# Kernel optimization log

Hardware: AMD Instinct MI355X
Metric: run time of the kernel (lower is better)

The kernel has to match this reference:

```python
import jax, jax.numpy as jnp
import numpy as np

I, H, NH, A = 128, 2048, 2, 4   # input_size, hidden_size, n_hidden, alpha_dim
K = 2 * A * A                   # per-position theta entries
B = 8192


def make_masks():
    # MADE sequential-ordering masks, identical to DART.create_masks
    inp = np.arange(I)
    degrees = [inp] + [np.arange(H) % (I - 1) for _ in range(NH + 1)] + [np.arange(I) - 1]
    masks = [(d1[:, None] >= d0[None, :]).astype(np.float32)
             for d0, d1 in zip(degrees[:-1], degrees[1:])]
    # last mask repeated per theta entry: repeat(1, K).view(-1, H) == row-repeat
    masks[-1] = np.repeat(masks[-1], K, axis=0)
    return [jnp.asarray(m) for m in masks]


def setup_inputs() -> dict:
    key = jax.random.key(0)
    ks = jax.random.split(key, 5)
    x = jax.random.normal(ks[0], (B, I), dtype=jnp.float32)

    def lin(k, out_dim, in_dim):
        kw, kb = jax.random.split(k)
        s = 1.0 / np.sqrt(in_dim)
        W = jax.random.uniform(kw, (out_dim, in_dim), minval=-s, maxval=s, dtype=jnp.float32)
        b = jax.random.uniform(kb, (out_dim,), minval=-s, maxval=s, dtype=jnp.float32)
        return W, b

    W0, b0 = lin(ks[1], H, I)
    W1, b1 = lin(ks[2], H, H)
    W2, b2 = lin(ks[3], H, H)
    W3, b3 = lin(ks[4], I * K, H)
    return dict(x=x, W0=W0, b0=b0, W1=W1, b1=b1, W2=W2, b2=b2, W3=W3, b3=b3)


def logexpmm(a, b):
    # log-domain matmul: out[..., i, j] = logsumexp_k(a[..., i, k] + b[..., k, j])
    return jax.nn.logsumexp(a[..., :, :, None] + b[..., None, :, :], axis=-2)


def reference(x, W0, b0, W1, b1, W2, b2, W3, b3):
    m = make_masks()
    h = jax.nn.relu(x @ (m[0] * W0).T + b0)
    h = jax.nn.relu(h @ (m[1] * W1).T + b1)
    h = jax.nn.relu(h @ (m[2] * W2).T + b2)
    theta = (h @ (m[3] * W3).T + b3).reshape(-1, I, 2, A, A)
    mu, alpha = theta[:, :, 0], theta[:, :, 1]  # (B, I, A, A)

    LOG2PI = float(np.log(2.0 * np.pi))
    xe = x[:, :, None, None]
    # Normal(mu, exp(alpha)).log_prob(x) - log(alpha_dim)
    logp = (-0.5 * ((xe - mu) * jnp.exp(-alpha)) ** 2
            - alpha - 0.5 * LOG2PI - jnp.log(jnp.float32(A)))

    first = logp[:, 0, 0:1]        # (B, 1, A)
    last = logp[:, -1, :, 0:1]     # (B, A, 1)
    inner = jnp.swapaxes(logp[:, 1:-1], 0, 1)  # (I-2, B, A, A)

    def step(carry, mtx):
        return logexpmm(carry, mtx), None

    prod, _ = jax.lax.scan(step, inner[0], inner[1:])
    return logexpmm(first, logexpmm(prod, last))  # (B, 1, 1)
```

## Files before the change

kernel.cpp:

```cpp
#include <hip/hip_runtime.h>
#include <hip/hip_bf16.h>
#include <cstdint>
#include <cstddef>

#define AS1 __attribute__((address_space(1)))
#define AS3 __attribute__((address_space(3)))

typedef __bf16 bf16x8  __attribute__((ext_vector_type(8)));
typedef float  floatx4 __attribute__((ext_vector_type(4)));

__device__ __forceinline__ void load_lds16(const void* g, void* l) {
    __builtin_amdgcn_global_load_lds((AS1 void*)g, (AS3 void*)l, 16, 0, 0);
}

__device__ __forceinline__ float fexp2(float x) { return __builtin_amdgcn_exp2f(x); }
__device__ __forceinline__ float flog2(float x) { return __builtin_amdgcn_logf(x); }

#define LOG2E 1.4426950408889634f
#define LN2   0.6931471805599453f
#define C0K   2.3052328943245633f

__device__ __forceinline__ float logp2(float xv, float mu, float al) {
    float e = fexp2(-al * LOG2E);
    float z = (xv - mu) * e;
    return (-0.5f * z * z - al - C0K) * LOG2E;
}
__device__ __forceinline__ float lse4(float a0, float a1, float a2, float a3) {
    float mx = fmaxf(fmaxf(a0, a1), fmaxf(a2, a3));
    return mx + flog2(fexp2(a0 - mx) + fexp2(a1 - mx) +
                      fexp2(a2 - mx) + fexp2(a3 - mx));
}
__device__ __forceinline__ void lmm4(const float* Aa, const float* Bb, float* D) {
#pragma unroll
    for (int r = 0; r < 4; ++r)
#pragma unroll
        for (int c = 0; c < 4; ++c)
            D[r * 4 + c] = lse4(Aa[r * 4 + 0] + Bb[0 * 4 + c],
                                Aa[r * 4 + 1] + Bb[1 * 4 + c],
                                Aa[r * 4 + 2] + Bb[2 * 4 + c],
                                Aa[r * 4 + 3] + Bb[3 * 4 + c]);
}

__device__ __forceinline__ int resp_s(int p) {
    return p < 272 ? p / 17 : 16 + ((p - 272) >> 4);
}
__device__ __forceinline__ int invp_s(int p) {
    if (p < 272) { int d = p / 17; int r = p - d * 17;
                   return r < 16 ? d + r * 127 : 2032 + d; }
    int d = 16 + ((p - 272) >> 4); int j = (p - 272) & 15;
    return d + j * 127;
}
__device__ __forceinline__ int cnt_le(int D) {
    return D < 16 ? (D + 1) * 17 : 272 + ((D - 15) << 4);
}

__global__ __launch_bounds__(256)
void prep_all(const float* __restrict__ x,  const float* __restrict__ W0,
              const float* __restrict__ W1, const float* __restrict__ W2,
              const float* __restrict__ W3,
              __bf16* __restrict__ xb,  __bf16* __restrict__ w0m,
              __bf16* __restrict__ w1m, __bf16* __restrict__ w2m,
              __bf16* __restrict__ w3m)
{
    __shared__ float lds[2048];
    const int blk = blockIdx.x;
    const int tid = threadIdx.x;
    const int t8  = tid * 8;

    if (blk < 640) {
        bf16x8 o;
        if (blk < 512) {
            size_t base = (size_t)blk * 2048 + t8;
            floatx4 a = *(const floatx4*)(x + base);
            floatx4 b = *(const floatx4*)(x + base + 4);
#pragma unroll
            for (int j = 0; j < 4; ++j) { o[j] = (__bf16)a[j]; o[4 + j] = (__bf16)b[j]; }
            *(bf16x8*)(xb + base) = o;
        } else {
            long idx = (long)(blk - 512) * 2048 + t8;
            int p_n = (int)(idx >> 7);
            int c   = (int)(idx & 127);
            int dg  = resp_s(p_n);
            const float* s = W0 + (long)invp_s(p_n) * 128 + c;
            floatx4 a = *(const floatx4*)s;
            floatx4 b = *(const floatx4*)(s + 4);
#pragma unroll
            for (int j = 0; j < 8; ++j) {
                float v = j < 4 ? a[j] : b[j - 4];
                o[j] = (__bf16)((dg >= c + j) ? v : 0.0f);
            }
            *(bf16x8*)(w0m + idx) = o;
        }
        return;
    }

    const float* srow; __bf16* drow; int deg_n; bool strict;
    if (blk < 2688) {
        int p_n = blk - 640;
        srow = W1 + (size_t)invp_s(p_n) * 2048; drow = w1m + (size_t)p_n * 2048;
        deg_n = resp_s(p_n); strict = false;
    } else if (blk < 4736) {
        int p_n = blk - 2688;
        srow = W2 + (size_t)invp_s(p_n) * 2048; drow = w2m + (size_t)p_n * 2048;
        deg_n = resp_s(p_n); strict = false;
    } else {
        int n = blk - 4736;
        srow = W3 + (size_t)n * 2048; drow = w3m + (size_t)n * 2048;
        deg_n = n >> 5; strict = true;
    }
    floatx4 a = *(const floatx4*)(srow + t8);
    floatx4 b = *(const floatx4*)(srow + t8 + 4);
    *(floatx4*)&lds[t8]     = a;
    *(floatx4*)&lds[t8 + 4] = b;
    __syncthreads();
    bf16x8 o;
#pragma unroll
    for (int j = 0; j < 8; ++j) {
        int p = t8 + j;
        float v = lds[invp_s(p)];
        int dg = resp_s(p);
        bool keep = strict ? (deg_n > dg) : (deg_n >= dg);
        o[j] = (__bf16)(keep ? v : 0.0f);
    }
    *(bf16x8*)(drow + t8) = o;
}

template <bool RELU, bool OBF16, bool TLAYOUT, bool PERMBIAS, int LMODE>
__global__ __launch_bounds__(256, 4)
void gemm_bt(const __bf16* __restrict__ A, const __bf16* __restrict__ Bw,
             const float* __restrict__ bias, void* __restrict__ Cout,
             int N, int K)
{
    __shared__ __align__(16) __bf16 lsA[128 * 64];
    __shared__ __align__(16) __bf16 lsB[128 * 64];
    const int tid  = threadIdx.x;
    const int wave = tid >> 6;
    const int lane = tid & 63;
    const int bm = blockIdx.x;
    const int bn = (gridDim.y - 1) - blockIdx.y;
    const int wm = wave >> 1, wn = wave & 1;

    const int r8 = lane >> 3;
    const int cb = (lane & 7) ^ r8;
    const __bf16* gsrc[8];
    __bf16* ldst[8];
#pragma unroll
    for (int t = 0; t < 8; ++t) {
        int j = wave * 8 + t;
        if (j < 16) {
            int row = bm * 128 + j * 8 + r8;
            gsrc[t] = A + (size_t)row * K + cb * 8;
            ldst[t] = lsA + j * 512;
        } else {
            int jj = j - 16;
            int row = bn * 128 + jj * 8 + r8;
            gsrc[t] = Bw + (size_t)row * K + cb * 8;
            ldst[t] = lsB + jj * 512;
        }
    }

    const int fr  = lane & 15;
    const int ks  = lane >> 4;
    const int sx  = fr & 7;
    const int sl0 = ((ks)     ^ sx) * 8;
    const int sl1 = ((4 + ks) ^ sx) * 8;
    const __bf16* arow[4];
    const __bf16* brow[4];
#pragma unroll
    for (int i = 0; i < 4; ++i) {
        arow[i] = lsA + (wm * 64 + i * 16 + fr) * 64;
        brow[i] = lsB + (wn * 64 + i * 16 + fr) * 64;
    }

    floatx4 acc[4][4];
    const floatx4 vzero = {0.f, 0.f, 0.f, 0.f};
#pragma unroll
    for (int mi = 0; mi < 4; ++mi)
#pragma unroll
        for (int ni = 0; ni < 4; ++ni) acc[mi][ni] = vzero;

    const int nk = K >> 6;
    int limit;
    if (LMODE == 0)      limit = (cnt_le(resp_s(bn * 128 + 127)) + 63) >> 6;
    else if (LMODE == 1) { int D = 4 * bn + 2; if (D > 126) D = 126;
                           limit = (cnt_le(D) + 63) >> 6; }
    else                 limit = (resp_s(bn * 128 + 127) + 64) >> 6;
    if (limit > nk) limit = nk;

    for (int it = 0; it < limit; ++it) {
        const int kt = it << 6;
        __syncthreads();
#pragma unroll
        for (int t = 0; t < 8; ++t)
            load_lds16((const void*)(gsrc[t] + kt), (void*)ldst[t]);
        __syncthreads();
        bf16x8 af[4], bf[4];
#pragma unroll
        for (int i = 0; i < 4; ++i) af[i] = *(const bf16x8*)(arow[i] + sl0);
#pragma unroll
        for (int i = 0; i < 4; ++i) bf[i] = *(const bf16x8*)(brow[i] + sl0);
#pragma unroll
        for (int mi = 0; mi < 4; ++mi)
#pragma unroll
            for (int ni = 0; ni < 4; ++ni)
                acc[mi][ni] = __builtin_amdgcn_mfma_f32_16x16x32_bf16(
                    af[mi], bf[ni], acc[mi][ni], 0, 0, 0);
#pragma unroll
        for (int i = 0; i < 4; ++i) af[i] = *(const bf16x8*)(arow[i] + sl1);
#pragma unroll
        for (int i = 0; i < 4; ++i) bf[i] = *(const bf16x8*)(brow[i] + sl1);
#pragma unroll
        for (int mi = 0; mi < 4; ++mi)
#pragma unroll
            for (int ni = 0; ni < 4; ++ni)
                acc[mi][ni] = __builtin_amdgcn_mfma_f32_16x16x32_bf16(
                    af[mi], bf[ni], acc[mi][ni], 0, 0, 0);
    }

    const int cn  = lane & 15;
    const int cr4 = (lane >> 4) * 4;
#pragma unroll
    for (int ni = 0; ni < 4; ++ni) {
        int col = bn * 128 + wn * 64 + ni * 16 + cn;
        float bv = bias[PERMBIAS ? invp_s(col) : col];
#pragma unroll
        for (int mi = 0; mi < 4; ++mi) {
            int row0 = bm * 128 + wm * 64 + mi * 16 + cr4;
#pragma unroll
            for (int q = 0; q < 4; ++q) {
                float v = acc[mi][ni][q] + bv;
                if (RELU) v = fmaxf(v, 0.f);
                if (TLAYOUT) {
                    size_t addr = (size_t)(bm * 2 + wm) * ((size_t)N * 64)
                                + (size_t)col * 64 + (mi * 16 + cr4 + q);
                    ((__bf16*)Cout)[addr] = (__bf16)v;
                } else if (OBF16) {
                    ((__bf16*)Cout)[(size_t)(row0 + q) * N + col] = (__bf16)v;
                } else {
                    ((float*)Cout)[(size_t)(row0 + q) * N + col] = v;
                }
            }
        }
    }
}

#define CFENCE() asm volatile("" ::: "memory")
#define BARX()  do { CFENCE(); __builtin_amdgcn_s_barrier(); CFENCE(); } while (0)
#define WVM2()  asm volatile("s_waitcnt vmcnt(2)" ::: "memory")
#define WVM0()  asm volatile("s_waitcnt vmcnt(0)" ::: "memory")
#define WLGK()  asm volatile("s_waitcnt lgkmcnt(0)" ::: "memory")

template <bool RELU, bool OBF16, bool TLAYOUT, bool PERMBIAS, int LMODE>
__global__ __launch_bounds__(512)
void gemm8p(const __bf16* __restrict__ A, const __bf16* __restrict__ Bw,
            const float* __restrict__ bias, void* __restrict__ Cout,
            int N, int K)
{
    __shared__ __align__(16) __bf16 ls[2 * 24576];
    const int tid  = threadIdx.x;
    const int wave = tid >> 6;
    const int lane = tid & 63;
    const int bm = blockIdx.x;
    const int bn = (gridDim.y - 1) - blockIdx.y;
    const int wm = wave >> 1, wn = wave & 1;

    const int l8 = lane >> 3;
    const int cb = (lane & 7) ^ l8;
    const __bf16* gA[2][2];  int dA[2][2];
    const __bf16* gB[2];     int dB[2];
#pragma unroll
    for (int h = 0; h < 2; ++h)
#pragma unroll
        for (int s = 0; s < 2; ++s) {
            int rt = h * 128 + wave * 16 + s * 8;
            gA[h][s] = A + (size_t)(bm * 256 + rt + l8) * K + cb * 8;
            dA[h][s] = rt * 64;
        }
#pragma unroll
    for (int s = 0; s < 2; ++s) {
        int rt = wave * 16 + s * 8;
        gB[s] = Bw + (size_t)(bn * 128 + rt + l8) * K + cb * 8;
        dB[s] = 16384 + rt * 64;
    }

#define STG_A(buf, kt) do { \
    load_lds16((const void*)(gA[0][0] + (kt)), (void*)(ls + (buf)*24576 + dA[0][0])); \
    load_lds16((const void*)(gA[0][1] + (kt)), (void*)(ls + (buf)*24576 + dA[0][1])); \
    load_lds16((const void*)(gA[1][0] + (kt)), (void*)(ls + (buf)*24576 + dA[1][0])); \
    load_lds16((const void*)(gA[1][1] + (kt)), (void*)(ls + (buf)*24576 + dA[1][1])); } while (0)
#define STG_B(buf, kt) do { \
    load_lds16((const void*)(gB[0] + (kt)), (void*)(ls + (buf)*24576 + dB[0])); \
    load_lds16((const void*)(gB[1] + (kt)), (void*)(ls + (buf)*24576 + dB[1])); } while (0)

    const int fr  = lane & 15;
    const int ks  = lane >> 4;
    const int sx  = fr & 7;
    const int sl0 = ((ks)     ^ sx) * 8;
    const int sl1 = ((4 + ks) ^ sx) * 8;
    int aoff[4], boff[4];
#pragma unroll
    for (int i = 0; i < 4; ++i) {
        aoff[i] = (wm * 64 + i * 16 + fr) * 64;
        boff[i] = 16384 + (wn * 64 + i * 16 + fr) * 64;
    }

    floatx4 acc[4][4];
    const floatx4 vzero = {0.f, 0.f, 0.f, 0.f};
#pragma unroll
    for (int mi = 0; mi < 4; ++mi)
#pragma unroll
        for (int ni = 0; ni < 4; ++ni) acc[mi][ni] = vzero;

    bf16x8 bfr[4][2], afr[2][2];

#define DSRD_B(buf) do { \
    _Pragma("unroll") \
    for (int ni = 0; ni < 4; ++ni) { \
        bfr[ni][0] = *(const bf16x8*)(ls + (buf)*24576 + boff[ni] + sl0); \
        bfr[ni][1] = *(const bf16x8*)(ls + (buf)*24576 + boff[ni] + sl1); } } while (0)
#define DSRD_A(buf, q) do { \
    _Pragma("unroll") \
    for (int j = 0; j < 2; ++j) { \
        afr[j][0] = *(const bf16x8*)(ls + (buf)*24576 + aoff[2*(q)+j] + sl0); \
        afr[j][1] = *(const bf16x8*)(ls + (buf)*24576 + aoff[2*(q)+j] + sl1); } } while (0)
#define MFMA16(q) do { \
    __builtin_amdgcn_s_setprio(1); \
    _Pragma("unroll") \
    for (int j = 0; j < 2; ++j) \
    _Pragma("unroll") \
    for (int ni = 0; ni < 4; ++ni) { \
        acc[2*(q)+j][ni] = __builtin_amdgcn_mfma_f32_16x16x32_bf16( \
            afr[j][0], bfr[ni][0], acc[2*(q)+j][ni], 0, 0, 0); \
        acc[2*(q)+j][ni] = __builtin_amdgcn_mfma_f32_16x16x32_bf16( \
            afr[j][1], bfr[ni][1], acc[2*(q)+j][ni], 0, 0, 0); } \
    __builtin_amdgcn_s_setprio(0); } while (0)

    const int nk = K >> 6;
    int limit;
    if (LMODE == 0)      limit = (cnt_le(resp_s(bn * 128 + 127)) + 63) >> 6;
    else if (LMODE == 1) { int D = 4 * bn + 2; if (D > 126) D = 126;
                           limit = (cnt_le(D) + 63) >> 6; }
    else                 limit = (resp_s(bn * 128 + 127) + 64) >> 6;
    if (limit > nk) limit = nk;
    const int NT = limit;

    STG_B(0, 0);
    STG_A(0, 0);
    if (NT > 1) { STG_B(1, 64); WVM2(); } else { WVM0(); }
    BARX();

    for (int t = 0; ; t += 2) {
        const int kt1 = (t + 1) << 6, kt2 = (t + 2) << 6, kt3 = (t + 3) << 6;
        const bool has1 = t + 1 < NT, has2 = t + 2 < NT, has3 = t + 3 < NT;

        DSRD_B(0);
        DSRD_A(0, 0);
        if (has1) STG_A(1, kt1);
        BARX(); WLGK();
        MFMA16(0);
        BARX();

        DSRD_A(0, 1);
        if (has2) STG_B(0, kt2);
        BARX(); WLGK();
        MFMA16(1);
        if (!has1) break;
        if (has2) WVM2(); else WVM0();
        BARX();

        DSRD_B(1);
        DSRD_A(1, 0);
        if (has2) STG_A(0, kt2);
        BARX(); WLGK();
        MFMA16(0);
        BARX();

        DSRD_A(1, 1);
        if (has3) STG_B(1, kt3);
        BARX(); WLGK();
        MFMA16(1);
        if (!has2) break;
        if (has3) WVM2(); else WVM0();
        BARX();
    }

    const int cn  = lane & 15;
    const int cr4 = (lane >> 4) * 4;
#pragma unroll
    for (int ni = 0; ni < 4; ++ni) {
        int col = bn * 128 + wn * 64 + ni * 16 + cn;
        float bv = bias[PERMBIAS ? invp_s(col) : col];
#pragma unroll
        for (int mi = 0; mi < 4; ++mi) {
            int row0 = bm * 256 + wm * 64 + mi * 16 + cr4;
#pragma unroll
            for (int q = 0; q < 4; ++q) {
                float v = acc[mi][ni][q] + bv;
                if (RELU) v = fmaxf(v, 0.f);
                if (TLAYOUT) {
                    size_t addr = (size_t)(bm * 4 + wm) * ((size_t)N * 64)
                                + (size_t)col * 64 + (mi * 16 + cr4 + q);
                    ((__bf16*)Cout)[addr] = (__bf16)v;
                } else if (OBF16) {
                    ((__bf16*)Cout)[(size_t)(row0 + q) * N + col] = (__bf16)v;
                } else {
                    ((float*)Cout)[(size_t)(row0 + q) * N + col] = v;
                }
            }
        }
    }
#undef STG_A
#undef STG_B
#undef DSRD_B
#undef DSRD_A
#undef MFMA16
}

__global__ __launch_bounds__(448)
void chain_all(const __bf16* __restrict__ th2,
               const float* __restrict__ x,
               float* __restrict__ out)
{
    __shared__ float xs[32 * 129];
    __shared__ float Pl[32 * 238];
    const int tid = threadIdx.x;
    const int blk = blockIdx.x;

    for (int idx = tid; idx < 4096; idx += 448) {
        int bl = idx >> 7, i = idx & 127;
        xs[bl * 129 + i] = x[(size_t)blk * 4096 + idx];
    }
    __syncthreads();

    const int s  = tid >> 5;
    const int bl = tid & 31;
    const int b64 = (blk & 1) * 32 + bl;
    const __bf16* tb = th2 + (size_t)(blk >> 1) * (4096 * 64) + b64;

    {
        const int i0 = 1 + s * 9;
        const __bf16* tp = tb + (size_t)i0 * 32 * 64;
        float M[4][4];
#pragma unroll
        for (int r = 0; r < 4; ++r)
#pragma unroll
            for (int c = 0; c < 4; ++c) M[r][c] = (r == c) ? 0.f : -1e30f;

        for (int ii = 0; ii < 9; ++ii) {
            float mu[16], al[16];
#pragma unroll
            for (int j = 0; j < 16; ++j) mu[j] = (float)tp[(size_t)j * 64];
#pragma unroll
            for (int j = 0; j < 16; ++j) al[j] = (float)tp[(size_t)(16 + j) * 64];
            float xv = xs[bl * 129 + i0 + ii];
            tp += 2048;
            float lp[16];
#pragma unroll
            for (int j = 0; j < 16; ++j) lp[j] = logp2(xv, mu[j], al[j]);
            float Mn[4][4];
#pragma unroll
            for (int r = 0; r < 4; ++r)
#pragma unroll
                for (int c = 0; c < 4; ++c)
                    Mn[r][c] = lse4(M[r][0] + lp[0 + c], M[r][1] + lp[4 + c],
                                    M[r][2] + lp[8 + c], M[r][3] + lp[12 + c]);
#pragma unroll
            for (int r = 0; r < 4; ++r)
#pragma unroll
                for (int c = 0; c < 4; ++c) M[r][c] = Mn[r][c];
        }
        float* pb = Pl + bl * 238 + s * 17;
#pragma unroll
        for (int r = 0; r < 4; ++r)
#pragma unroll
            for (int c = 0; c < 4; ++c) pb[r * 4 + c] = M[r][c];
    }
    __syncthreads();

    float Q[16];
    if (tid < 224) {
        const float* base = Pl + bl * 238;
        lmm4(base + (2 * s) * 17, base + (2 * s + 1) * 17, Q);
    }
    __syncthreads();
    if (tid < 224) {
        float* dst = Pl + bl * 238 + s * 17;
#pragma unroll
        for (int e = 0; e < 16; ++e) dst[e] = Q[e];
    }
    __syncthreads();

    if (tid < 32) {
        const float* base = Pl + tid * 238;
        float M[16], T[16];
#pragma unroll
        for (int e = 0; e < 16; ++e) M[e] = base[e];
#pragma unroll
        for (int j = 1; j < 7; ++j) {
            lmm4(M, base + j * 17, T);
#pragma unroll
            for (int e = 0; e < 16; ++e) M[e] = T[e];
        }
        const int bb64 = (blk & 1) * 32 + tid;
        const __bf16* tbb = th2 + (size_t)(blk >> 1) * (4096 * 64) + bb64;
        float x0 = xs[tid * 129 + 0];
        float xl = xs[tid * 129 + 127];
        float last[4], t4[4], f4[4];
#pragma unroll
        for (int c = 0; c < 4; ++c)
            last[c] = logp2(xl, (float)tbb[(size_t)(4064 + c * 4) * 64],
                                (float)tbb[(size_t)(4064 + 16 + c * 4) * 64]);
#pragma unroll
        for (int r = 0; r < 4; ++r)
            t4[r] = lse4(M[r * 4 + 0] + last[0], M[r * 4 + 1] + last[1],
                         M[r * 4 + 2] + last[2], M[r * 4 + 3] + last[3]);
#pragma unroll
        for (int r = 0; r < 4; ++r)
            f4[r] = logp2(x0, (float)tbb[(size_t)r * 64],
                              (float)tbb[(size_t)(16 + r) * 64]);
        out[blk * 32 + tid] = LN2 * lse4(f4[0] + t4[0], f4[1] + t4[1],
                                         f4[2] + t4[2], f4[3] + t4[3]);
    }
}

extern "C" void kernel_launch(void* const* d_in, const int* in_sizes, int n_in,
                              void* d_out, int out_size, void* d_ws, size_t ws_size,
                              hipStream_t stream)
{
    (void)in_sizes; (void)n_in; (void)out_size; (void)ws_size;
    const float* x  = (const float*)d_in[0];
    const float* W0 = (const float*)d_in[1];
    const float* b0 = (const float*)d_in[2];
    const float* W1 = (const float*)d_in[3];
    const float* b1 = (const float*)d_in[4];
    const float* W2 = (const float*)d_in[5];
    const float* b2 = (const float*)d_in[6];
    const float* W3 = (const float*)d_in[7];
    const float* b3 = (const float*)d_in[8];

    char* ws = (char*)d_ws;
    const size_t MB = 1024 * 1024;
    __bf16* h2  = (__bf16*)(ws + 0);
    __bf16* xb  = (__bf16*)(ws + 32 * MB);
    __bf16* w0m = (__bf16*)(ws + 34 * MB);
    __bf16* w1m = (__bf16*)(ws + 35 * MB);
    __bf16* w2m = (__bf16*)(ws + 43 * MB);
    __bf16* th  = (__bf16*)(ws + 0);
    __bf16* w3m = (__bf16*)(ws + 64 * MB);
    __bf16* h1  = (__bf16*)(ws + 80 * MB);
    __bf16* h3  = h1;

    prep_all<<<8832, 256, 0, stream>>>(x, W0, W1, W2, W3, xb, w0m, w1m, w2m, w3m);

    gemm_bt<true, true, false, true, 2><<<dim3(64, 16), 256, 0, stream>>>(
        xb, w0m, b0, h1, 2048, 128);
    gemm8p<true, true, false, true, 0><<<dim3(32, 16), 512, 0, stream>>>(
        h1, w1m, b1, h2, 2048, 2048);
    gemm8p<true, true, false, true, 0><<<dim3(32, 16), 512, 0, stream>>>(
        h2, w2m, b2, h3, 2048, 2048);
    gemm_bt<false, false, true, false, 1><<<dim3(64, 32), 256, 0, stream>>>(
        h3, w3m, b3, th, 4096, 2048);

    chain_all<<<256, 448, 0, stream>>>(th, x, (float*)d_out);
}
```

Before: 316.9 us.

## Store theta in position-major per-row layout for vectorized chain loads

Changes the transposed theta layout written by the last GEMM epilogue so that each batch row's 32 theta values for a position are contiguous. The chain kernel then reads them with four 16-byte vector loads instead of 32 strided scalar bf16 loads. The producer's stores become more scattered (per-lane stride of 32 elements), which may cost write coalescing in the GEMM epilogue.

```diff
diff --git a/kernel.cpp b/kernel.cpp
--- a/kernel.cpp
+++ b/kernel.cpp
@@ -232,7 +232,8 @@
                 if (RELU) v = fmaxf(v, 0.f);
                 if (TLAYOUT) {
                     size_t addr = (size_t)(bm * 2 + wm) * ((size_t)N * 64)
-                                + (size_t)col * 64 + (mi * 16 + cr4 + q);
+                                + (size_t)(col >> 5) * 2048
+                                + (size_t)(mi * 16 + cr4 + q) * 32 + (col & 31);
                     ((__bf16*)Cout)[addr] = (__bf16)v;
                 } else if (OBF16) {
                     ((__bf16*)Cout)[(size_t)(row0 + q) * N + col] = (__bf16)v;
@@ -399,7 +400,8 @@
                 if (RELU) v = fmaxf(v, 0.f);
                 if (TLAYOUT) {
                     size_t addr = (size_t)(bm * 4 + wm) * ((size_t)N * 64)
-                                + (size_t)col * 64 + (mi * 16 + cr4 + q);
+                                + (size_t)(col >> 5) * 2048
+                                + (size_t)(mi * 16 + cr4 + q) * 32 + (col & 31);
                     ((__bf16*)Cout)[addr] = (__bf16)v;
                 } else if (OBF16) {
                     ((__bf16*)Cout)[(size_t)(row0 + q) * N + col] = (__bf16)v;
@@ -435,11 +437,11 @@
     const int s  = tid >> 5;
     const int bl = tid & 31;
     const int b64 = (blk & 1) * 32 + bl;
-    const __bf16* tb = th2 + (size_t)(blk >> 1) * (4096 * 64) + b64;
+    const __bf16* tb = th2 + (size_t)(blk >> 1) * 262144 + (size_t)b64 * 32;
 
     {
         const int i0 = 1 + s * 9;
-        const __bf16* tp = tb + (size_t)i0 * 32 * 64;
+        const __bf16* tp = tb + (size_t)i0 * 2048;
         float M[4][4];
 #pragma unroll
         for (int r = 0; r < 4; ++r)
@@ -447,11 +449,16 @@
             for (int c = 0; c < 4; ++c) M[r][c] = (r == c) ? 0.f : -1e30f;
 
         for (int ii = 0; ii < 9; ++ii) {
+            bf16x8 v0 = *(const bf16x8*)(tp);
+            bf16x8 v1 = *(const bf16x8*)(tp + 8);
+            bf16x8 v2 = *(const bf16x8*)(tp + 16);
+            bf16x8 v3 = *(const bf16x8*)(tp + 24);
             float mu[16], al[16];
 #pragma unroll
-            for (int j = 0; j < 16; ++j) mu[j] = (float)tp[(size_t)j * 64];
-#pragma unroll
-            for (int j = 0; j < 16; ++j) al[j] = (float)tp[(size_t)(16 + j) * 64];
+            for (int j = 0; j < 8; ++j) {
+                mu[j] = (float)v0[j]; mu[8 + j] = (float)v1[j];
+                al[j] = (float)v2[j]; al[8 + j] = (float)v3[j];
+            }
             float xv = xs[bl * 129 + i0 + ii];
             tp += 2048;
             float lp[16];
@@ -502,22 +509,21 @@
             for (int e = 0; e < 16; ++e) M[e] = T[e];
         }
         const int bb64 = (blk & 1) * 32 + tid;
-        const __bf16* tbb = th2 + (size_t)(blk >> 1) * (4096 * 64) + bb64;
+        const __bf16* tbb = th2 + (size_t)(blk >> 1) * 262144 + (size_t)bb64 * 32;
         float x0 = xs[tid * 129 + 0];
         float xl = xs[tid * 129 + 127];
         float last[4], t4[4], f4[4];
 #pragma unroll
         for (int c = 0; c < 4; ++c)
-            last[c] = logp2(xl, (float)tbb[(size_t)(4064 + c * 4) * 64],
-                                (float)tbb[(size_t)(4064 + 16 + c * 4) * 64]);
+            last[c] = logp2(xl, (float)tbb[(size_t)127 * 2048 + c * 4],
+                                (float)tbb[(size_t)127 * 2048 + 16 + c * 4]);
 #pragma unroll
         for (int r = 0; r < 4; ++r)
             t4[r] = lse4(M[r * 4 + 0] + last[0], M[r * 4 + 1] + last[1],
                          M[r * 4 + 2] + last[2], M[r * 4 + 3] + last[3]);
 #pragma unroll
         for (int r = 0; r < 4; ++r)
-            f4[r] = logp2(x0, (float)tbb[(size_t)r * 64],
-                              (float)tbb[(size_t)(16 + r) * 64]);
+            f4[r] = logp2(x0, (float)tbb[r], (float)tbb[16 + r]);
         out[blk * 32 + tid] = LN2 * lse4(f4[0] + t4[0], f4[1] + t4[1],
                                          f4[2] + t4[2], f4[3] + t4[3]);
     }
```

After: 314.6 us. No clear change (-0.8%).
